# Kernel optimization log

Hardware: AMD Instinct MI355X
Metric: run time of the kernel (lower is better)

Reference implementation:

```python
import jax, jax.numpy as jnp
import numpy as np

NUM_CLUSTERS = 16
CHANNELS = 256
UPDATE_RATE = 0.2
# channels % num_clusters == 0 -> all cluster capacities equal
_BASE = CHANNELS // NUM_CLUSTERS
_REM = CHANNELS % NUM_CLUSTERS
CLUSTER_SIZES = jnp.asarray([_BASE + 1] * _REM + [_BASE] * (NUM_CLUSTERS - _REM), dtype=jnp.int32)


def _cdist(a, b):
    # euclidean pairwise distance, batched over leading dims
    d2 = (jnp.sum(a * a, -1)[..., :, None]
          + jnp.sum(b * b, -1)[..., None, :]
          - 2.0 * (a @ jnp.swapaxes(b, -1, -2)))
    return jnp.sqrt(jnp.clip(d2, 0.0))


def _fps(D, k):
    # farthest point sampling given full [N,N] distance matrix
    start = jnp.argmax(D.sum(1))
    def step(min_d, _):
        far = jnp.argmax(min_d)
        return jnp.minimum(min_d, D[far]), far
    _, rest = jax.lax.scan(step, D[start], None, length=k - 1)
    return jnp.concatenate([start[None], rest])


def _capacity_assign(D, sizes):
    # greedy fixed-capacity assignment, sequential over channels
    order = jnp.argsort(D, axis=1)  # [C, K] cluster preference per channel
    def step(counts, row):
        avail = counts[row] < sizes[row]
        chosen = row[jnp.argmax(avail)]  # first available preference
        return counts.at[chosen].add(1), chosen
    _, assign = jax.lax.scan(step, jnp.zeros(sizes.shape[0], jnp.int32), order)
    return assign


def setup_inputs() -> dict:
    key = jax.random.key(0)
    k1, k2 = jax.random.split(key)
    features = jax.random.normal(k1, (8, CHANNELS, 64, 256), dtype=jnp.float32)
    pos_emb_batch = jax.random.normal(k2, (8, CHANNELS, 3), dtype=jnp.float32)
    return {"features": features, "pos_emb_batch": pos_emb_batch}


def reference(features, pos_emb_batch):
    b, c, nw, df = features.shape
    K = NUM_CLUSTERS
    pos = pos_emb_batch[0]                                   # [C, 3] (module's pos_emb buffer)
    # _initialize_centers: FPS over electrode positions
    centers = pos[_fps(_cdist(pos, pos), K)]                 # [K, 3]
    # _find_farthest_channels (euclidean): FPS over flattened features per batch
    ff = features.reshape(b, c, -1)
    Db = _cdist(ff, ff)                                      # [b, C, C]
    sel = jax.vmap(lambda D: _fps(D, K))(Db)                 # [b, K]
    # _cluster_euclidean_temp: nearest temp center per channel
    center_coords = pos_emb_batch[jnp.arange(b)[:, None], sel]      # [b, K, 3]
    temp_assign = jnp.argmin(_cdist(pos_emb_batch, center_coords), -1)  # [b, C]
    # per-cluster mean of positions over the whole batch
    flat_a = temp_assign.reshape(-1)
    flat_p = pos_emb_batch.reshape(-1, 3)
    sums = jax.ops.segment_sum(flat_p, flat_a, num_segments=K)
    cnts = jax.ops.segment_sum(jnp.ones(flat_a.shape, jnp.float32), flat_a, num_segments=K)
    avg = jnp.where(cnts[:, None] > 0, sums / jnp.maximum(cnts, 1.0)[:, None], 0.0)
    # match old centers to batch-average temp centers and EMA update
    matching = jnp.argmin(_cdist(centers, avg), axis=1)
    centers = (1.0 - UPDATE_RATE) * centers + UPDATE_RATE * avg[matching]
    # capacity-constrained final assignment
    return _capacity_assign(_cdist(pos, centers), CLUSTER_SIZES)
```

## Files before the change

kernel.cpp:

```cpp
#include <hip/hip_runtime.h>

#define NB 8
#define NC 256
#define DF 16384
#define KCL 16
#define SPLITS 16
#define KC (DF / SPLITS)
#define BK 32
#define ITERS (KC / BK)
#define NPAIR 3
#define GEMM_BLOCKS (NPAIR * 2 * NB * SPLITS)

typedef _Float16 half8 __attribute__((ext_vector_type(8)));
typedef _Float16 half4_t __attribute__((ext_vector_type(4)));
typedef float floatx4 __attribute__((ext_vector_type(4)));

__device__ const int TItab[NPAIR] = {0,0,1};
__device__ const int TJtab[NPAIR] = {0,1,1};

__device__ __forceinline__ int argmax256(float v, float* sv, int* si) {
  int t = threadIdx.x;
  sv[t] = v; si[t] = t;
  __syncthreads();
  #pragma unroll
  for (int s = 128; s >= 1; s >>= 1) {
    if (t < s) {
      float a = sv[t], b = sv[t + s];
      int ia = si[t], ib = si[t + s];
      if (b > a || (b == a && ib < ia)) { sv[t] = b; si[t] = ib; }
    }
    __syncthreads();
  }
  int r = si[0];
  __syncthreads();
  return r;
}

__device__ __forceinline__ int argmax512p(float v, float* sv, int* si) {
  int t = threadIdx.x;
  sv[t] = v; si[t] = t;
  __syncthreads();
  #pragma unroll
  for (int s = 256; s >= 1; s >>= 1) {
    if (t < s) {
      float a = sv[t], b = sv[t + s];
      int ia = si[t], ib = si[t + s];
      if (b > a || (b == a && ib < ia)) { sv[t] = b; si[t] = ib; }
    }
    __syncthreads();
  }
  int r = si[0];
  __syncthreads();
  return r;
}

__global__ __launch_bounds__(512, 3) void k_gemm_pre(const float* __restrict__ ff,
                                                     const float* __restrict__ pe,
                                                     float* __restrict__ Pp,
                                                     float* __restrict__ centers0,
                                                     float* __restrict__ rs) {
  __shared__ _Float16 Ah[128][40];
  __shared__ _Float16 Al[128][40];
  __shared__ _Float16 Bh[64][40];
  __shared__ _Float16 Bl[64][40];

  const int bid = blockIdx.x;
  const int tid = threadIdx.x;

  if (bid == GEMM_BLOCKS) {
    float* sm = (float*)&Ah[0][0];
    float* px = sm;        float* py = sm + 256;
    float* pz = sm + 512;  float* pn = sm + 768;
    float* sv = sm + 1024; int*   si = (int*)(sm + 1536);
    int* fpsIdx = (int*)(sm + 2048);
    const int t = tid;
    for (int i = t; i < NB * NC; i += 512) rs[i] = 0.f;
    const bool valid = t < NC;
    float x = 0.f, y = 0.f, z = 0.f, n = 0.f;
    if (valid) {
      x = pe[t * 3 + 0]; y = pe[t * 3 + 1]; z = pe[t * 3 + 2];
      n = x * x + y * y + z * z;
      px[t] = x; py[t] = y; pz[t] = z; pn[t] = n;
    }
    __syncthreads();
    float rsum = -3.4e38f;
    if (valid) {
      rsum = 0.f;
      for (int j = 0; j < NC; ++j) {
        float dot = x * px[j] + y * py[j] + z * pz[j];
        rsum += sqrtf(fmaxf(n + pn[j] - 2.f * dot, 0.f));
      }
    }
    int start = argmax512p(rsum, sv, si);
    if (t == 0) fpsIdx[0] = start;
    float mind = -3.4e38f;
    if (valid) {
      float dot0 = x * px[start] + y * py[start] + z * pz[start];
      mind = sqrtf(fmaxf(n + pn[start] - 2.f * dot0, 0.f));
    }
    for (int it = 1; it < KCL; ++it) {
      int far = argmax512p(mind, sv, si);
      if (t == 0) fpsIdx[it] = far;
      if (valid) {
        float dot = x * px[far] + y * py[far] + z * pz[far];
        mind = fminf(mind, sqrtf(fmaxf(n + pn[far] - 2.f * dot, 0.f)));
      }
    }
    __syncthreads();
    if (t < KCL) {
      int p = fpsIdx[t];
      centers0[t * 3 + 0] = px[p];
      centers0[t * 3 + 1] = py[p];
      centers0[t * 3 + 2] = pz[p];
    }
    return;
  }

  const int tc = bid % 6;
  const int b  = (bid / 6) & 7;
  const int sp = bid / 48;
  const int pair = tc >> 1, ch = tc & 1;
  const int ti = TItab[pair], tj = TJtab[pair];
  const bool diag = (ti == tj);

  const int wave = tid >> 6, lane = tid & 63;
  const int wr = wave >> 1, wc = wave & 1;
  const int lrow = lane & 15, q = lane >> 4;

  const int srA = tid >> 2, scA = (tid & 3) * 8;
  const int srB = tid >> 3, scB = (tid & 7) * 4;
  const float* gA = ff + ((size_t)(b * NC + ti * 128 + srA)) * DF + sp * KC + scA;
  const float* gB = ff + ((size_t)(b * NC + tj * 128 + ch * 64 + srB)) * DF + sp * KC + scB;

  floatx4 a1[2][2], a2[2][2], a3[2][2];
  #pragma unroll
  for (int i = 0; i < 2; ++i)
    #pragma unroll
    for (int j = 0; j < 2; ++j) { a1[i][j] = (floatx4)0.f; a2[i][j] = (floatx4)0.f; a3[i][j] = (floatx4)0.f; }

  float4 ra0 = *(const float4*)(gA), ra1 = *(const float4*)(gA + 4);
  float4 rb = make_float4(0.f, 0.f, 0.f, 0.f);
  if (!diag) rb = *(const float4*)(gB);
  gA += BK; gB += BK;

  for (int it = 0; it < ITERS; ++it) {
    float fa[8] = {ra0.x, ra0.y, ra0.z, ra0.w, ra1.x, ra1.y, ra1.z, ra1.w};
    half8 ah, al;
    #pragma unroll
    for (int e = 0; e < 8; ++e) {
      _Float16 h = (_Float16)fa[e];
      ah[e] = h;
      al[e] = (_Float16)(fa[e] - (float)h);
    }
    half4_t bh4, bl4;
    if (!diag) {
      float fb[4] = {rb.x, rb.y, rb.z, rb.w};
      #pragma unroll
      for (int e = 0; e < 4; ++e) {
        _Float16 h = (_Float16)fb[e];
        bh4[e] = h;
        bl4[e] = (_Float16)(fb[e] - (float)h);
      }
    }
    __syncthreads();
    *(half8*)&Ah[srA][scA] = ah;
    *(half8*)&Al[srA][scA] = al;
    if (!diag) {
      *(half4_t*)&Bh[srB][scB] = bh4;
      *(half4_t*)&Bl[srB][scB] = bl4;
    }
    __syncthreads();
    if (it + 1 < ITERS) {
      ra0 = *(const float4*)(gA); ra1 = *(const float4*)(gA + 4);
      if (!diag) rb = *(const float4*)(gB);
      gA += BK; gB += BK;
    }
    const _Float16* bhp = diag ? &Ah[ch * 64][0] : &Bh[0][0];
    const _Float16* blp = diag ? &Al[ch * 64][0] : &Bl[0][0];
    half8 af[2], lf[2];
    #pragma unroll
    for (int i = 0; i < 2; ++i) {
      af[i] = *(const half8*)&Ah[wr * 32 + i * 16 + lrow][q * 8];
      lf[i] = *(const half8*)&Al[wr * 32 + i * 16 + lrow][q * 8];
    }
    #pragma unroll
    for (int j = 0; j < 2; ++j) {
      half8 bhf = *(const half8*)(bhp + (wc * 32 + j * 16 + lrow) * 40 + q * 8);
      half8 blf = *(const half8*)(blp + (wc * 32 + j * 16 + lrow) * 40 + q * 8);
      #pragma unroll
      for (int i = 0; i < 2; ++i) {
        a1[i][j] = __builtin_amdgcn_mfma_f32_16x16x32_f16(af[i], bhf, a1[i][j], 0, 0, 0);
        a2[i][j] = __builtin_amdgcn_mfma_f32_16x16x32_f16(af[i], blf, a2[i][j], 0, 0, 0);
        a3[i][j] = __builtin_amdgcn_mfma_f32_16x16x32_f16(lf[i], bhf, a3[i][j], 0, 0, 0);
      }
    }
  }

  float* Pb = Pp + (size_t)(sp * NB + b) * NC * NC;
  #pragma unroll
  for (int i = 0; i < 2; ++i) {
    int grow = ti * 128 + wr * 32 + i * 16 + q * 4;
    #pragma unroll
    for (int j = 0; j < 2; ++j) {
      int gcol = tj * 128 + ch * 64 + wc * 32 + j * 16 + lrow;
      float4 v;
      v.x = a1[i][j][0] + a2[i][j][0] + a3[i][j][0];
      v.y = a1[i][j][1] + a2[i][j][1] + a3[i][j][1];
      v.z = a1[i][j][2] + a2[i][j][2] + a3[i][j][2];
      v.w = a1[i][j][3] + a2[i][j][3] + a3[i][j][3];
      Pb[(size_t)(grow + 0) * NC + gcol] = v.x;
      Pb[(size_t)(grow + 1) * NC + gcol] = v.y;
      Pb[(size_t)(grow + 2) * NC + gcol] = v.z;
      Pb[(size_t)(grow + 3) * NC + gcol] = v.w;
      if (!diag) *(float4*)&Pb[(size_t)gcol * NC + grow] = v;
    }
  }
}

__global__ __launch_bounds__(256) void k_formD(const float* __restrict__ Pp,
                                               float* __restrict__ Db,
                                               float* __restrict__ rs) {
  __shared__ float dg_s[NC];
  const int t = threadIdx.x;
  const int b = blockIdx.x >> 5, i0 = (blockIdx.x & 31) * 8;
  float s = 0.f;
  #pragma unroll
  for (int sp = 0; sp < SPLITS; ++sp)
    s += Pp[((size_t)(sp * NB + b) * NC + t) * NC + t];
  dg_s[t] = s;
  __syncthreads();
  float colsum = 0.f;
  for (int ii = 0; ii < 8; ++ii) {
    int i = i0 + ii;
    float acc = 0.f;
    #pragma unroll
    for (int sp = 0; sp < SPLITS; ++sp)
      acc += Pp[((size_t)(sp * NB + b) * NC + i) * NC + t];
    float d2 = dg_s[i] + dg_s[t] - 2.f * acc;
    float d = sqrtf(fmaxf(d2, 0.f));
    Db[((size_t)b * NC + i) * NC + t] = d;
    colsum += d;
  }
  atomicAdd(&rs[b * NC + t], colsum);
}

__global__ __launch_bounds__(256) void k_fps_b(const float* __restrict__ Db,
                                               const float* __restrict__ rs,
                                               const float* __restrict__ pe,
                                               float* __restrict__ ccoord) {
  int b = blockIdx.x, t = threadIdx.x;
  const float* D = Db + (size_t)b * NC * NC;
  __shared__ float sv[NC]; __shared__ int si[NC];
  __shared__ int fpsIdx[KCL];
  int start = argmax256(rs[b * NC + t], sv, si);
  if (t == 0) fpsIdx[0] = start;
  float mind = D[start * NC + t];
  for (int it = 1; it < KCL; ++it) {
    int far = argmax256(mind, sv, si);
    if (t == 0) fpsIdx[it] = far;
    mind = fminf(mind, D[far * NC + t]);
  }
  __syncthreads();
  if (t < KCL) {
    int p = fpsIdx[t];
    ccoord[(b * KCL + t) * 3 + 0] = pe[(b * NC + p) * 3 + 0];
    ccoord[(b * KCL + t) * 3 + 1] = pe[(b * NC + p) * 3 + 1];
    ccoord[(b * KCL + t) * 3 + 2] = pe[(b * NC + p) * 3 + 2];
  }
}

__global__ __launch_bounds__(256) void k_final(const float* __restrict__ pe,
                                               const float* __restrict__ ccoord,
                                               const float* __restrict__ centers0,
                                               int* __restrict__ outp) {
  __shared__ float cc[NB * KCL * 3];
  __shared__ float cn[NB * KCL];
  __shared__ float sums[KCL][3];
  __shared__ int cnts[KCL];
  __shared__ float avg[KCL][3];
  __shared__ float an[KCL];
  __shared__ float c0[KCL * 3];
  __shared__ float c1x[KCL], c1y[KCL], c1z[KCL], c1n[KCL];
  __shared__ int order[NC][KCL];
  int t = threadIdx.x;
  for (int i = t; i < NB * KCL * 3; i += 256) cc[i] = ccoord[i];
  if (t < KCL * 3) c0[t] = centers0[t];
  if (t < KCL) { sums[t][0] = 0.f; sums[t][1] = 0.f; sums[t][2] = 0.f; cnts[t] = 0; }
  __syncthreads();
  if (t < NB * KCL) {
    float x = cc[t * 3], y = cc[t * 3 + 1], z = cc[t * 3 + 2];
    cn[t] = x * x + y * y + z * z;
  }
  __syncthreads();
  for (int b = 0; b < NB; ++b) {
    int p = b * NC + t;
    float x = pe[p * 3], y = pe[p * 3 + 1], z = pe[p * 3 + 2];
    float n = x * x + y * y + z * z;
    float best = 3.4e38f; int bi = 0;
    #pragma unroll
    for (int k = 0; k < KCL; ++k) {
      int c = b * KCL + k;
      float dot = x * cc[c * 3] + y * cc[c * 3 + 1] + z * cc[c * 3 + 2];
      float d2 = fmaxf(n + cn[c] - 2.f * dot, 0.f);
      if (d2 < best) { best = d2; bi = k; }
    }
    atomicAdd(&sums[bi][0], x);
    atomicAdd(&sums[bi][1], y);
    atomicAdd(&sums[bi][2], z);
    atomicAdd(&cnts[bi], 1);
  }
  __syncthreads();
  if (t < KCL) {
    float c = (float)cnts[t];
    float inv = 1.f / fmaxf(c, 1.f);
    float ax = (cnts[t] > 0) ? sums[t][0] * inv : 0.f;
    float ay = (cnts[t] > 0) ? sums[t][1] * inv : 0.f;
    float az = (cnts[t] > 0) ? sums[t][2] * inv : 0.f;
    avg[t][0] = ax; avg[t][1] = ay; avg[t][2] = az;
    an[t] = ax * ax + ay * ay + az * az;
  }
  __syncthreads();
  if (t < KCL) {
    float x = c0[t * 3], y = c0[t * 3 + 1], z = c0[t * 3 + 2];
    float n = x * x + y * y + z * z;
    float best = 3.4e38f; int bi = 0;
    #pragma unroll
    for (int j = 0; j < KCL; ++j) {
      float dot = x * avg[j][0] + y * avg[j][1] + z * avg[j][2];
      float d2 = fmaxf(n + an[j] - 2.f * dot, 0.f);
      if (d2 < best) { best = d2; bi = j; }
    }
    float nx = 0.8f * x + 0.2f * avg[bi][0];
    float ny = 0.8f * y + 0.2f * avg[bi][1];
    float nz = 0.8f * z + 0.2f * avg[bi][2];
    c1x[t] = nx; c1y[t] = ny; c1z[t] = nz;
    c1n[t] = nx * nx + ny * ny + nz * nz;
  }
  __syncthreads();
  {
    float x = pe[t * 3], y = pe[t * 3 + 1], z = pe[t * 3 + 2];
    float n = x * x + y * y + z * z;
    float v[KCL];
    #pragma unroll
    for (int k = 0; k < KCL; ++k) {
      float dot = x * c1x[k] + y * c1y[k] + z * c1z[k];
      v[k] = fmaxf(n + c1n[k] - 2.f * dot, 0.f);
    }
    bool used[KCL];
    #pragma unroll
    for (int k = 0; k < KCL; ++k) used[k] = false;
    for (int r = 0; r < KCL; ++r) {
      float best = 3.4e38f; int bi = 0;
      #pragma unroll
      for (int j = 0; j < KCL; ++j) {
        if (!used[j] && v[j] < best) { best = v[j]; bi = j; }
      }
      order[t][r] = bi;
      used[bi] = true;
    }
  }
  __syncthreads();
  if (t < 64) {
    int cnt = 0;
    int cur = (t < KCL) ? order[0][t] : 0;
    for (int i = 0; i < NC; ++i) {
      int nxt = (t < KCL && i + 1 < NC) ? order[i + 1][t] : 0;
      int ccur = __shfl(cnt, cur);
      bool avail = (t < KCL) && (ccur < 16);
      unsigned long long m = __ballot(avail);
      int chosen;
      if (m != 0ull) {
        int rank = __ffsll((unsigned long long)m) - 1;
        chosen = __shfl(cur, rank);
      } else {
        chosen = __shfl(cur, 0);
      }
      if (t == chosen) cnt++;
      if (t == 0) outp[i] = chosen;
      cur = nxt;
    }
  }
}

extern "C" void kernel_launch(void* const* d_in, const int* in_sizes, int n_in,
                              void* d_out, int out_size, void* d_ws, size_t ws_size,
                              hipStream_t stream) {
  (void)in_sizes; (void)n_in; (void)out_size; (void)ws_size;
  const float* features = (const float*)d_in[0];
  const float* pe = (const float*)d_in[1];
  char* ws = (char*)d_ws;
  float* Pp       = (float*)(ws);
  float* Db       = (float*)(ws + 33554432);
  float* rs       = (float*)(ws + 35651584);
  float* centers0 = (float*)(ws + 35659776);
  float* ccoord   = (float*)(ws + 35660288);
  int*   outp     = (int*)d_out;

  hipLaunchKernelGGL(k_gemm_pre, dim3(GEMM_BLOCKS + 1), dim3(512), 0, stream,
                     features, pe, Pp, centers0, rs);
  hipLaunchKernelGGL(k_formD, dim3(256), dim3(256), 0, stream, Pp, Db, rs);
  hipLaunchKernelGGL(k_fps_b, dim3(NB), dim3(256), 0, stream, Db, rs, pe, ccoord);
  hipLaunchKernelGGL(k_final, dim3(1), dim3(256), 0, stream, pe, ccoord, centers0, outp);
}
```

Measured before the change: 335.8 us.

## Drop LDS staging in Gram GEMM, reduce splits with atomics, fuse distance into FPS

The GEMM now loads fp32 operands straight from global memory into registers in MFMA fragment layout, skipping LDS staging and its barriers. The three split-fp16 accumulators are merged into one. Split-K partial products are combined with float atomicAdds into a single zeroed Gram buffer instead of a 16-way partial buffer. The formD kernel is removed and the per-batch FPS kernel builds distances and row sums from the Gram matrix on the fly. This cuts the large partial-buffer writes and reads and one launch, at the cost of uncoalesced global loads, atomic contention, and a slower single-block-per-batch FPS that loops over 256 rows.

```diff
diff --git a/kernel.cpp b/kernel.cpp
--- a/kernel.cpp
+++ b/kernel.cpp
@@ -12,7 +12,6 @@
 #define GEMM_BLOCKS (NPAIR * 2 * NB * SPLITS)
 
 typedef _Float16 half8 __attribute__((ext_vector_type(8)));
-typedef _Float16 half4_t __attribute__((ext_vector_type(4)));
 typedef float floatx4 __attribute__((ext_vector_type(4)));
 
 __device__ const int TItab[NPAIR] = {0,0,1};
@@ -54,27 +53,32 @@
   return r;
 }
 
-__global__ __launch_bounds__(512, 3) void k_gemm_pre(const float* __restrict__ ff,
+__device__ __forceinline__ void cvt8(const float4 v0, const float4 v1,
+                                     half8& h, half8& l) {
+  float f[8] = {v0.x, v0.y, v0.z, v0.w, v1.x, v1.y, v1.z, v1.w};
+  #pragma unroll
+  for (int e = 0; e < 8; ++e) {
+    _Float16 hh = (_Float16)f[e];
+    h[e] = hh;
+    l[e] = (_Float16)(f[e] - (float)hh);
+  }
+}
+
+__global__ __launch_bounds__(512, 4) void k_gemm_pre(const float* __restrict__ ff,
                                                      const float* __restrict__ pe,
-                                                     float* __restrict__ Pp,
-                                                     float* __restrict__ centers0,
-                                                     float* __restrict__ rs) {
-  __shared__ _Float16 Ah[128][40];
-  __shared__ _Float16 Al[128][40];
-  __shared__ _Float16 Bh[64][40];
-  __shared__ _Float16 Bl[64][40];
+                                                     float* __restrict__ G,
+                                                     float* __restrict__ centers0) {
+  __shared__ float sm[2064];
 
   const int bid = blockIdx.x;
   const int tid = threadIdx.x;
 
   if (bid == GEMM_BLOCKS) {
-    float* sm = (float*)&Ah[0][0];
     float* px = sm;        float* py = sm + 256;
     float* pz = sm + 512;  float* pn = sm + 768;
     float* sv = sm + 1024; int*   si = (int*)(sm + 1536);
-    int* fpsIdx = (int*)(sm + 2048);
+    __shared__ int fpsIdx[KCL];
     const int t = tid;
-    for (int i = t; i < NB * NC; i += 512) rs[i] = 0.f;
     const bool valid = t < NC;
     float x = 0.f, y = 0.f, z = 0.f, n = 0.f;
     if (valid) {
@@ -127,138 +131,87 @@
   const int wr = wave >> 1, wc = wave & 1;
   const int lrow = lane & 15, q = lane >> 4;
 
-  const int srA = tid >> 2, scA = (tid & 3) * 8;
-  const int srB = tid >> 3, scB = (tid & 7) * 4;
-  const float* gA = ff + ((size_t)(b * NC + ti * 128 + srA)) * DF + sp * KC + scA;
-  const float* gB = ff + ((size_t)(b * NC + tj * 128 + ch * 64 + srB)) * DF + sp * KC + scB;
-
-  floatx4 a1[2][2], a2[2][2], a3[2][2];
+  const float* base = ff + (size_t)b * NC * DF + sp * KC + q * 8;
+  const float* pA0 = base + (size_t)(ti * 128 + wr * 32 +  0 + lrow) * DF;
+  const float* pA1 = base + (size_t)(ti * 128 + wr * 32 + 16 + lrow) * DF;
+  const float* pB0 = base + (size_t)(tj * 128 + ch * 64 + wc * 32 +  0 + lrow) * DF;
+  const float* pB1 = base + (size_t)(tj * 128 + ch * 64 + wc * 32 + 16 + lrow) * DF;
+
+  floatx4 acc[2][2];
   #pragma unroll
   for (int i = 0; i < 2; ++i)
     #pragma unroll
-    for (int j = 0; j < 2; ++j) { a1[i][j] = (floatx4)0.f; a2[i][j] = (floatx4)0.f; a3[i][j] = (floatx4)0.f; }
-
-  float4 ra0 = *(const float4*)(gA), ra1 = *(const float4*)(gA + 4);
-  float4 rb = make_float4(0.f, 0.f, 0.f, 0.f);
-  if (!diag) rb = *(const float4*)(gB);
-  gA += BK; gB += BK;
+    for (int j = 0; j < 2; ++j) acc[i][j] = (floatx4)0.f;
+
+  float4 va00 = *(const float4*)(pA0), va01 = *(const float4*)(pA0 + 4);
+  float4 va10 = *(const float4*)(pA1), va11 = *(const float4*)(pA1 + 4);
+  float4 vb00 = *(const float4*)(pB0), vb01 = *(const float4*)(pB0 + 4);
+  float4 vb10 = *(const float4*)(pB1), vb11 = *(const float4*)(pB1 + 4);
+  pA0 += BK; pA1 += BK; pB0 += BK; pB1 += BK;
 
   for (int it = 0; it < ITERS; ++it) {
-    float fa[8] = {ra0.x, ra0.y, ra0.z, ra0.w, ra1.x, ra1.y, ra1.z, ra1.w};
-    half8 ah, al;
-    #pragma unroll
-    for (int e = 0; e < 8; ++e) {
-      _Float16 h = (_Float16)fa[e];
-      ah[e] = h;
-      al[e] = (_Float16)(fa[e] - (float)h);
-    }
-    half4_t bh4, bl4;
-    if (!diag) {
-      float fb[4] = {rb.x, rb.y, rb.z, rb.w};
+    half8 af[2], lf[2], bh[2], bl[2];
+    cvt8(va00, va01, af[0], lf[0]);
+    cvt8(va10, va11, af[1], lf[1]);
+    cvt8(vb00, vb01, bh[0], bl[0]);
+    cvt8(vb10, vb11, bh[1], bl[1]);
+    if (it + 1 < ITERS) {
+      va00 = *(const float4*)(pA0); va01 = *(const float4*)(pA0 + 4);
+      va10 = *(const float4*)(pA1); va11 = *(const float4*)(pA1 + 4);
+      vb00 = *(const float4*)(pB0); vb01 = *(const float4*)(pB0 + 4);
+      vb10 = *(const float4*)(pB1); vb11 = *(const float4*)(pB1 + 4);
+      pA0 += BK; pA1 += BK; pB0 += BK; pB1 += BK;
+    }
+    #pragma unroll
+    for (int i = 0; i < 2; ++i)
       #pragma unroll
-      for (int e = 0; e < 4; ++e) {
-        _Float16 h = (_Float16)fb[e];
-        bh4[e] = h;
-        bl4[e] = (_Float16)(fb[e] - (float)h);
-      }
-    }
-    __syncthreads();
-    *(half8*)&Ah[srA][scA] = ah;
-    *(half8*)&Al[srA][scA] = al;
-    if (!diag) {
-      *(half4_t*)&Bh[srB][scB] = bh4;
-      *(half4_t*)&Bl[srB][scB] = bl4;
-    }
-    __syncthreads();
-    if (it + 1 < ITERS) {
-      ra0 = *(const float4*)(gA); ra1 = *(const float4*)(gA + 4);
-      if (!diag) rb = *(const float4*)(gB);
-      gA += BK; gB += BK;
-    }
-    const _Float16* bhp = diag ? &Ah[ch * 64][0] : &Bh[0][0];
-    const _Float16* blp = diag ? &Al[ch * 64][0] : &Bl[0][0];
-    half8 af[2], lf[2];
-    #pragma unroll
-    for (int i = 0; i < 2; ++i) {
-      af[i] = *(const half8*)&Ah[wr * 32 + i * 16 + lrow][q * 8];
-      lf[i] = *(const half8*)&Al[wr * 32 + i * 16 + lrow][q * 8];
-    }
-    #pragma unroll
-    for (int j = 0; j < 2; ++j) {
-      half8 bhf = *(const half8*)(bhp + (wc * 32 + j * 16 + lrow) * 40 + q * 8);
-      half8 blf = *(const half8*)(blp + (wc * 32 + j * 16 + lrow) * 40 + q * 8);
-      #pragma unroll
-      for (int i = 0; i < 2; ++i) {
-        a1[i][j] = __builtin_amdgcn_mfma_f32_16x16x32_f16(af[i], bhf, a1[i][j], 0, 0, 0);
-        a2[i][j] = __builtin_amdgcn_mfma_f32_16x16x32_f16(af[i], blf, a2[i][j], 0, 0, 0);
-        a3[i][j] = __builtin_amdgcn_mfma_f32_16x16x32_f16(lf[i], bhf, a3[i][j], 0, 0, 0);
-      }
-    }
-  }
-
-  float* Pb = Pp + (size_t)(sp * NB + b) * NC * NC;
+      for (int j = 0; j < 2; ++j) {
+        acc[i][j] = __builtin_amdgcn_mfma_f32_16x16x32_f16(af[i], bh[j], acc[i][j], 0, 0, 0);
+        acc[i][j] = __builtin_amdgcn_mfma_f32_16x16x32_f16(af[i], bl[j], acc[i][j], 0, 0, 0);
+        acc[i][j] = __builtin_amdgcn_mfma_f32_16x16x32_f16(lf[i], bh[j], acc[i][j], 0, 0, 0);
+      }
+  }
+
+  float* Gb = G + (size_t)b * NC * NC;
   #pragma unroll
   for (int i = 0; i < 2; ++i) {
     int grow = ti * 128 + wr * 32 + i * 16 + q * 4;
     #pragma unroll
     for (int j = 0; j < 2; ++j) {
       int gcol = tj * 128 + ch * 64 + wc * 32 + j * 16 + lrow;
-      float4 v;
-      v.x = a1[i][j][0] + a2[i][j][0] + a3[i][j][0];
-      v.y = a1[i][j][1] + a2[i][j][1] + a3[i][j][1];
-      v.z = a1[i][j][2] + a2[i][j][2] + a3[i][j][2];
-      v.w = a1[i][j][3] + a2[i][j][3] + a3[i][j][3];
-      Pb[(size_t)(grow + 0) * NC + gcol] = v.x;
-      Pb[(size_t)(grow + 1) * NC + gcol] = v.y;
-      Pb[(size_t)(grow + 2) * NC + gcol] = v.z;
-      Pb[(size_t)(grow + 3) * NC + gcol] = v.w;
-      if (!diag) *(float4*)&Pb[(size_t)gcol * NC + grow] = v;
-    }
-  }
-}
-
-__global__ __launch_bounds__(256) void k_formD(const float* __restrict__ Pp,
-                                               float* __restrict__ Db,
-                                               float* __restrict__ rs) {
+      #pragma unroll
+      for (int r = 0; r < 4; ++r)
+        atomicAdd(&Gb[(size_t)(grow + r) * NC + gcol], acc[i][j][r]);
+      if (!diag) {
+        #pragma unroll
+        for (int r = 0; r < 4; ++r)
+          atomicAdd(&Gb[(size_t)gcol * NC + grow + r], acc[i][j][r]);
+      }
+    }
+  }
+}
+
+__global__ __launch_bounds__(256) void k_fps(const float* __restrict__ G,
+                                             const float* __restrict__ pe,
+                                             float* __restrict__ ccoord) {
+  int b = blockIdx.x, t = threadIdx.x;
+  const float* Gb = G + (size_t)b * NC * NC;
   __shared__ float dg_s[NC];
-  const int t = threadIdx.x;
-  const int b = blockIdx.x >> 5, i0 = (blockIdx.x & 31) * 8;
-  float s = 0.f;
-  #pragma unroll
-  for (int sp = 0; sp < SPLITS; ++sp)
-    s += Pp[((size_t)(sp * NB + b) * NC + t) * NC + t];
-  dg_s[t] = s;
-  __syncthreads();
-  float colsum = 0.f;
-  for (int ii = 0; ii < 8; ++ii) {
-    int i = i0 + ii;
-    float acc = 0.f;
-    #pragma unroll
-    for (int sp = 0; sp < SPLITS; ++sp)
-      acc += Pp[((size_t)(sp * NB + b) * NC + i) * NC + t];
-    float d2 = dg_s[i] + dg_s[t] - 2.f * acc;
-    float d = sqrtf(fmaxf(d2, 0.f));
-    Db[((size_t)b * NC + i) * NC + t] = d;
-    colsum += d;
-  }
-  atomicAdd(&rs[b * NC + t], colsum);
-}
-
-__global__ __launch_bounds__(256) void k_fps_b(const float* __restrict__ Db,
-                                               const float* __restrict__ rs,
-                                               const float* __restrict__ pe,
-                                               float* __restrict__ ccoord) {
-  int b = blockIdx.x, t = threadIdx.x;
-  const float* D = Db + (size_t)b * NC * NC;
   __shared__ float sv[NC]; __shared__ int si[NC];
   __shared__ int fpsIdx[KCL];
-  int start = argmax256(rs[b * NC + t], sv, si);
+  dg_s[t] = Gb[(size_t)t * NC + t];
+  __syncthreads();
+  float dgt = dg_s[t];
+  float rs = 0.f;
+  for (int i = 0; i < NC; ++i)
+    rs += sqrtf(fmaxf(dg_s[i] + dgt - 2.f * Gb[(size_t)i * NC + t], 0.f));
+  int start = argmax256(rs, sv, si);
   if (t == 0) fpsIdx[0] = start;
-  float mind = D[start * NC + t];
+  float mind = sqrtf(fmaxf(dg_s[start] + dgt - 2.f * Gb[(size_t)start * NC + t], 0.f));
   for (int it = 1; it < KCL; ++it) {
     int far = argmax256(mind, sv, si);
     if (t == 0) fpsIdx[it] = far;
-    mind = fminf(mind, D[far * NC + t]);
+    mind = fminf(mind, sqrtf(fmaxf(dg_s[far] + dgt - 2.f * Gb[(size_t)far * NC + t], 0.f)));
   }
   __syncthreads();
   if (t < KCL) {
@@ -389,16 +342,14 @@
   const float* features = (const float*)d_in[0];
   const float* pe = (const float*)d_in[1];
   char* ws = (char*)d_ws;
-  float* Pp       = (float*)(ws);
-  float* Db       = (float*)(ws + 33554432);
-  float* rs       = (float*)(ws + 35651584);
-  float* centers0 = (float*)(ws + 35659776);
-  float* ccoord   = (float*)(ws + 35660288);
+  float* G        = (float*)(ws);
+  float* centers0 = (float*)(ws + 2097152);
+  float* ccoord   = (float*)(ws + 2097664);
   int*   outp     = (int*)d_out;
 
+  hipMemsetAsync(G, 0, (size_t)NB * NC * NC * sizeof(float), stream);
   hipLaunchKernelGGL(k_gemm_pre, dim3(GEMM_BLOCKS + 1), dim3(512), 0, stream,
-                     features, pe, Pp, centers0, rs);
-  hipLaunchKernelGGL(k_formD, dim3(256), dim3(256), 0, stream, Pp, Db, rs);
-  hipLaunchKernelGGL(k_fps_b, dim3(NB), dim3(256), 0, stream, Db, rs, pe, ccoord);
+                     features, pe, G, centers0);
+  hipLaunchKernelGGL(k_fps, dim3(NB), dim3(256), 0, stream, G, pe, ccoord);
   hipLaunchKernelGGL(k_final, dim3(1), dim3(256), 0, stream, pe, ccoord, centers0, outp);
 }
```

New measurement: 439.4 us. +30.8%, slower.
